# Performance work log

Hardware: AMD Instinct MI355X
Metric: run time of the kernel (lower is better)

## Reference

```python
import jax, jax.numpy as jnp
import numpy as np
from jax import lax

B, N, C, H = 8, 1024, 384, 6
D = C // H
SCALE = D ** -0.5
EPS = 1e-5


def setup_inputs() -> dict:
    key = jax.random.key(0)
    ks = jax.random.split(key, 10)
    s = 0.02
    return {
        "x": jax.random.normal(ks[0], (B, N, C), jnp.float32),
        "w_qkv": jax.random.normal(ks[1], (3 * C, C), jnp.float32) * s,
        "w_proj": jax.random.normal(ks[2], (C, C), jnp.float32) * s,
        "b_proj": jax.random.normal(ks[3], (C,), jnp.float32) * s,
        "w_kq": jax.random.normal(ks[4], (H, 1, 3, 3), jnp.float32) * 0.1,   # depthwise (groups=H)
        "b_kq": jax.random.normal(ks[5], (H,), jnp.float32) * 0.1,
        "w_head": jax.random.normal(ks[6], (H, H, 1, 1), jnp.float32) * 0.1,  # 1x1 head-mixing conv
        "b_head": jax.random.normal(ks[7], (H,), jnp.float32) * 0.1,
        "gn_w": jnp.ones((H,), jnp.float32),
        "gn_b": jnp.zeros((H,), jnp.float32),
    }


def reference(x, w_qkv, w_proj, b_proj, w_kq, b_kq, w_head, b_head, gn_w, gn_b):
    # qkv projection (torch Linear: y = x @ W.T)
    qkv = (x @ w_qkv.T).reshape(B, N, 3, H, D).transpose(2, 0, 3, 1, 4)  # [3,B,H,N,D]
    q, k, v = qkv[0], qkv[1], qkv[2]

    # attention logits [B,H,N,N]
    logits = jnp.einsum("bhnd,bhmd->bhnm", q, k) * SCALE

    # depthwise (groups=H) 3x3 conv over the NxN logit map
    logits = lax.conv_general_dilated(
        logits, w_kq, window_strides=(1, 1), padding=((1, 1), (1, 1)),
        dimension_numbers=("NCHW", "OIHW", "NCHW"), feature_group_count=H,
    ) + b_kq[None, :, None, None]

    attn = jax.nn.softmax(logits, axis=-1)

    # 1x1 conv mixing heads
    attn = jnp.einsum("oh,bhnm->bonm", w_head[:, :, 0, 0], attn) + b_head[None, :, None, None]

    # GroupNorm(num_groups=H, channels=H): per (b, head) stats over NxN
    mean = attn.mean(axis=(2, 3), keepdims=True)
    var = ((attn - mean) ** 2).mean(axis=(2, 3), keepdims=True)
    attn = (attn - mean) * lax.rsqrt(var + EPS)
    attn = attn * gn_w[None, :, None, None] + gn_b[None, :, None, None]

    out = jnp.einsum("bhnm,bhmd->bhnd", attn, v)
    out = out.transpose(0, 2, 1, 3).reshape(B, N, C)
    return out @ w_proj.T + b_proj
```

## Files before the change

### kernel.cpp

```cpp
#include <hip/hip_runtime.h>

typedef unsigned short u16;
typedef __attribute__((ext_vector_type(8))) short short8;
typedef __attribute__((ext_vector_type(4))) float f32x4;

#define MFMA(a, b, c) __builtin_amdgcn_mfma_f32_16x16x32_bf16((a), (b), (c), 0, 0, 0)

__device__ inline float bf2f(u16 u) {
  union { unsigned int i; float f; } w; w.i = ((unsigned int)u) << 16; return w.f;
}
__device__ inline u16 f2bf(float x) {
  union { float f; unsigned int i; } u; u.f = x;
  unsigned int r = u.i + 0x7fffu + ((u.i >> 16) & 1u);
  return (u16)(r >> 16);
}
__device__ inline unsigned int pk2(float a, float b) {
  return (unsigned int)f2bf(a) | ((unsigned int)f2bf(b) << 16);
}
__device__ inline void unpack8(uint4 v, float* f) {
  union { unsigned int i; float g; } c;
  c.i = v.x << 16;          f[0] = c.g;
  c.i = v.x & 0xffff0000u;  f[1] = c.g;
  c.i = v.y << 16;          f[2] = c.g;
  c.i = v.y & 0xffff0000u;  f[3] = c.g;
  c.i = v.z << 16;          f[4] = c.g;
  c.i = v.z & 0xffff0000u;  f[5] = c.g;
  c.i = v.w << 16;          f[6] = c.g;
  c.i = v.w & 0xffff0000u;  f[7] = c.g;
}

static const size_t SZ_QKV = (size_t)48 * 1024 * 64 * 2;
static const size_t SZ_MAP = (size_t)48 * 1024 * 1024 * 2;
static const size_t OFF_Q  = 0;
static const size_t OFF_K  = OFF_Q + SZ_QKV;
static const size_t OFF_VT = OFF_K + SZ_QKV;
static const size_t OFF_UG = OFF_VT + SZ_QKV;
static const size_t OFF_QM = OFF_UG + SZ_MAP;
static const size_t OFF_OT = OFF_QM + SZ_MAP;
static const size_t OFF_ST = OFF_OT + SZ_QKV;
static const size_t OFF_CS = OFF_ST + 896;

__global__ __launch_bounds__(256, 3) void k_qkv(const float* __restrict__ x,
                                                const float* __restrict__ w,
                                                u16* __restrict__ qb,
                                                u16* __restrict__ kb,
                                                u16* __restrict__ vT,
                                                float* __restrict__ colsum) {
  __shared__ u16 SH[16384];
  u16* As = SH;
  u16* Bs = SH + 8192;
  const int t = threadIdx.x;
  const int m0 = blockIdx.x * 128;
  const int n0 = blockIdx.y * 128;
  const int wave = t >> 6, lane = t & 63;
  const int wm = (wave & 1) * 64, wn = (wave >> 1) * 64;
  const int fr = lane & 15;
  const int fk = (lane >> 4) * 8;
  f32x4 acc[4][4] = {};
  for (int k0 = 0; k0 < 384; k0 += 64) {
#pragma unroll
    for (int i = 0; i < 4; ++i) {
      int e = (i * 256 + t) * 8;
      int row = e >> 6, col = e & 63;
      const float* xp = &x[(size_t)(m0 + row) * 384 + k0 + col];
      const float* wp = &w[(size_t)(n0 + row) * 384 + k0 + col];
      float4 a0 = *(const float4*)xp, a1 = *(const float4*)(xp + 4);
      uint4 av; av.x = pk2(a0.x, a0.y); av.y = pk2(a0.z, a0.w);
      av.z = pk2(a1.x, a1.y); av.w = pk2(a1.z, a1.w);
      *(uint4*)&As[e] = av;
      float4 b0 = *(const float4*)wp, b1 = *(const float4*)(wp + 4);
      uint4 bv; bv.x = pk2(b0.x, b0.y); bv.y = pk2(b0.z, b0.w);
      bv.z = pk2(b1.x, b1.y); bv.w = pk2(b1.z, b1.w);
      *(uint4*)&Bs[e] = bv;
    }
    __syncthreads();
#pragma unroll
    for (int ks = 0; ks < 2; ++ks) {
      const int ko = ks * 32 + fk;
      short8 a[4], b[4];
#pragma unroll
      for (int mi = 0; mi < 4; ++mi) a[mi] = *(const short8*)&As[(wm + mi * 16 + fr) * 64 + ko];
#pragma unroll
      for (int ni = 0; ni < 4; ++ni) b[ni] = *(const short8*)&Bs[(wn + ni * 16 + fr) * 64 + ko];
#pragma unroll
      for (int mi = 0; mi < 4; ++mi)
#pragma unroll
        for (int ni = 0; ni < 4; ++ni) acc[mi][ni] = MFMA(a[mi], b[ni], acc[mi][ni]);
    }
    __syncthreads();
  }
  u16* st = &SH[wave * 4096];
  const int gcb = n0 + wn;
  const int s = gcb / 384;
  const int remb = gcb - s * 384;
  const int h = remb >> 6;
#pragma unroll
  for (int mi = 0; mi < 4; ++mi)
#pragma unroll
    for (int ni = 0; ni < 4; ++ni)
#pragma unroll
      for (int r = 0; r < 4; ++r) {
        int rl = mi * 16 + (lane >> 4) * 4 + r;
        int cl = ni * 16 + fr;
        u16 val = f2bf(acc[mi][ni][r]);
        if (s == 2) st[cl * 64 + rl] = val;
        else        st[rl * 64 + cl] = val;
      }
  const int gm0 = m0 + wm;
  const int b_ = gm0 >> 10;
  const size_t base = (size_t)(b_ * 6 + h) << 16;
  const int nloc = gm0 & 1023;
  const int r8 = lane >> 3, c8 = (lane & 7) * 8;
#pragma unroll
  for (int i = 0; i < 8; ++i) {
    int lrow = i * 8 + r8;
    uint4 v = *(const uint4*)&st[lrow * 64 + c8];
    if (s == 0)      *(uint4*)&qb[base + (size_t)(nloc + lrow) * 64 + c8] = v;
    else if (s == 1) *(uint4*)&kb[base + (size_t)(nloc + lrow) * 64 + c8] = v;
    else             *(uint4*)&vT[base + (size_t)lrow * 1024 + nloc + c8] = v;
  }
  if (s == 2) {
#pragma unroll
    for (int ni = 0; ni < 4; ++ni) {
      float p = 0.f;
#pragma unroll
      for (int mi = 0; mi < 4; ++mi)
#pragma unroll
        for (int r = 0; r < 4; ++r) p += bf2f(f2bf(acc[mi][ni][r]));
      p += __shfl_xor(p, 16, 64);
      p += __shfl_xor(p, 32, 64);
      if ((lane >> 4) == 0)
        atomicAdd(&colsum[(b_ * 6 + h) * 64 + ni * 16 + fr], p);
    }
  }
}

__global__ __launch_bounds__(256) void k_qkconv(const u16* __restrict__ qb,
                                                const u16* __restrict__ kb,
                                                const float* __restrict__ w_kq,
                                                u16* __restrict__ Qb) {
  __shared__ u16 Sr[16 * 1040];
  __shared__ u16 Qs[16 * 68];
  __shared__ u16 Ks[64 * 68];
  __shared__ float red[4];
  const int t = threadIdx.x;
  const int bid = blockIdx.x;
  const int b_ = bid & 7;
  const int rest = bid >> 3;
  const int h = rest % 6;
  const int band = rest / 6;
  const int bh = b_ * 6 + h;
  const int n0 = band * 14;
  const int wave = t >> 6, lane = t & 63;
  const int fr = lane & 15, quad = lane >> 4;

  if (t < 128) {
    int i = t >> 3, c8 = (t & 7) * 8;
    int g = n0 - 1 + i;
    uint4 val = make_uint4(0u, 0u, 0u, 0u);
    if (g >= 0 && g < 1024)
      val = *(const uint4*)&qb[((size_t)bh << 16) + (size_t)g * 64 + c8];
    *(uint4*)&Qs[i * 68 + c8] = val;
  }
  if (t < 16) { Sr[t * 1040 + 7] = 0; Sr[t * 1040 + 1032] = 0; }
  const u16* kp = kb + ((size_t)bh << 16);
  uint4 kreg0 = *(const uint4*)&kp[(size_t)(t >> 3) * 64 + (t & 7) * 8];
  uint4 kreg1 = *(const uint4*)&kp[(size_t)(32 + (t >> 3)) * 64 + (t & 7) * 8];

  for (int c = 0; c < 16; ++c) {
    __syncthreads();
    *(uint4*)&Ks[(t >> 3) * 68 + (t & 7) * 8] = kreg0;
    *(uint4*)&Ks[((t >> 3) + 32) * 68 + (t & 7) * 8] = kreg1;
    if (c < 15) {
      const size_t ro = (size_t)(c + 1) * 64 * 64;
      kreg0 = *(const uint4*)&kp[ro + (size_t)(t >> 3) * 64 + (t & 7) * 8];
      kreg1 = *(const uint4*)&kp[ro + (size_t)(32 + (t >> 3)) * 64 + (t & 7) * 8];
    }
    __syncthreads();
    f32x4 acc = {};
#pragma unroll
    for (int ks = 0; ks < 2; ++ks) {
      short8 a = *(const short8*)&Qs[fr * 68 + ks * 32 + quad * 8];
      short8 bfr = *(const short8*)&Ks[(wave * 16 + fr) * 68 + ks * 32 + quad * 8];
      acc = MFMA(a, bfr, acc);
    }
#pragma unroll
    for (int r = 0; r < 4; ++r)
      Sr[(quad * 4 + r) * 1040 + 8 + c * 64 + wave * 16 + fr] = f2bf(acc[r] * 0.125f);
  }
  __syncthreads();

  float wv[9];
#pragma unroll
  for (int i = 0; i < 9; ++i) wv[i] = w_kq[h * 9 + i];
  const int half = t >> 7;
  const int m0 = (t & 127) * 8;
  for (int pass = 0; pass < 7; ++pass) {
    int rr = pass * 2 + half;
    float o8[8];
#pragma unroll
    for (int j = 0; j < 8; ++j) o8[j] = 0.f;
#pragma unroll
    for (int i = 0; i < 3; ++i) {
      const u16* rowp = &Sr[(rr + i) * 1040 + 8];
      float left = bf2f(rowp[m0 - 1]);
      float md[8];
      unpack8(*(const uint4*)&rowp[m0], md);
      float right = bf2f(rowp[m0 + 8]);
      float w0 = wv[i * 3 + 0], w1 = wv[i * 3 + 1], w2 = wv[i * 3 + 2];
      o8[0] += w0 * left + w1 * md[0] + w2 * md[1];
#pragma unroll
      for (int j = 1; j < 7; ++j) o8[j] += w0 * md[j - 1] + w1 * md[j] + w2 * md[j + 1];
      o8[7] += w0 * md[6] + w1 * md[7] + w2 * right;
    }
    float mx = o8[0];
#pragma unroll
    for (int j = 1; j < 8; ++j) mx = fmaxf(mx, o8[j]);
    for (int off = 32; off; off >>= 1) mx = fmaxf(mx, __shfl_xor(mx, off, 64));
    if (lane == 0) red[t >> 6] = mx;
    __syncthreads();
    float rmax = fmaxf(red[half * 2], red[half * 2 + 1]);
    __syncthreads();
    float e8[8], s = 0.f;
#pragma unroll
    for (int j = 0; j < 8; ++j) { e8[j] = __expf(o8[j] - rmax); s += e8[j]; }
    for (int off = 32; off; off >>= 1) s += __shfl_xor(s, off, 64);
    if (lane == 0) red[t >> 6] = s;
    __syncthreads();
    float rsum = red[half * 2] + red[half * 2 + 1];
    __syncthreads();
    float scale = 1024.f / rsum;
    int n = n0 + rr;
    if (n < 1024) {
      unsigned int pk[4];
#pragma unroll
      for (int jj = 0; jj < 4; ++jj)
        pk[jj] = pk2(e8[2 * jj] * scale - 1.f, e8[2 * jj + 1] * scale - 1.f);
      *(uint4*)&Qb[((size_t)bh << 20) + (size_t)n * 1024 + m0] = make_uint4(pk[0], pk[1], pk[2], pk[3]);
    }
  }
}

__global__ __launch_bounds__(256) void k_pvmix(const u16* __restrict__ Qm,
                                               const u16* __restrict__ vT,
                                               const float* __restrict__ wh,
                                               float* __restrict__ Ug,
                                               float* __restrict__ stats) {
  __shared__ u16 SH[2 * 64 * 72];
  u16* Am = SH;
  u16* Vm = SH + 64 * 72;
  const int t = threadIdx.x;
  const int bid = blockIdx.x;
  const int b_ = bid & 7;
  const int sidx = bid >> 3;
  const int n0 = (sidx / 6) * 64;
  const int o = sidx % 6;
  const int bo = b_ * 6 + o;
  const int wave = t >> 6, lane = t & 63;
  const int fr = lane & 15, quad = lane >> 4;
  const int srow = t >> 3, smg8 = (t & 7) * 8;
  float wo[6];
#pragma unroll
  for (int hh = 0; hh < 6; ++hh) wo[hh] = wh[o * 6 + hh];
  const size_t qbase = ((size_t)(b_ * 6)) << 20;
  const u16* vp = vT + ((size_t)bo << 16);
  uint4 qpre[2][6];
  uint4 vpre[2];
  {
    const int m = smg8;
#pragma unroll
    for (int i = 0; i < 2; ++i)
#pragma unroll
      for (int hh = 0; hh < 6; ++hh)
        qpre[i][hh] = *(const uint4*)&Qm[qbase + (((size_t)hh) << 20) +
                                         (size_t)(n0 + i * 32 + srow) * 1024 + m];
    vpre[0] = *(const uint4*)&vp[(size_t)srow * 1024 + m];
    vpre[1] = *(const uint4*)&vp[(size_t)(32 + srow) * 1024 + m];
  }
  f32x4 acc[4] = {};
  float s1 = 0.f, s2 = 0.f;
  for (int mc = 0; mc < 16; ++mc) {
    __syncthreads();
#pragma unroll
    for (int i = 0; i < 2; ++i) {
      float mix[8] = {0.f, 0.f, 0.f, 0.f, 0.f, 0.f, 0.f, 0.f};
#pragma unroll
      for (int hh = 0; hh < 6; ++hh) {
        float qf[8];
        unpack8(qpre[i][hh], qf);
        float w = wo[hh];
#pragma unroll
        for (int j = 0; j < 8; ++j) mix[j] += w * qf[j];
      }
#pragma unroll
      for (int j = 0; j < 8; ++j) { s1 += mix[j]; s2 += mix[j] * mix[j]; }
      uint4 pk4;
      pk4.x = pk2(mix[0], mix[1]); pk4.y = pk2(mix[2], mix[3]);
      pk4.z = pk2(mix[4], mix[5]); pk4.w = pk2(mix[6], mix[7]);
      *(uint4*)&Am[(i * 32 + srow) * 72 + smg8] = pk4;
    }
    *(uint4*)&Vm[srow * 72 + smg8] = vpre[0];
    *(uint4*)&Vm[(32 + srow) * 72 + smg8] = vpre[1];
    if (mc < 15) {
      const int m = (mc + 1) * 64 + smg8;
#pragma unroll
      for (int i = 0; i < 2; ++i)
#pragma unroll
        for (int hh = 0; hh < 6; ++hh)
          qpre[i][hh] = *(const uint4*)&Qm[qbase + (((size_t)hh) << 20) +
                                           (size_t)(n0 + i * 32 + srow) * 1024 + m];
      vpre[0] = *(const uint4*)&vp[(size_t)srow * 1024 + m];
      vpre[1] = *(const uint4*)&vp[(size_t)(32 + srow) * 1024 + m];
    }
    __syncthreads();
#pragma unroll
    for (int ks = 0; ks < 2; ++ks) {
      short8 a = *(const short8*)&Am[(wave * 16 + fr) * 72 + ks * 32 + quad * 8];
#pragma unroll
      for (int ni = 0; ni < 4; ++ni) {
        short8 b = *(const short8*)&Vm[(ni * 16 + fr) * 72 + ks * 32 + quad * 8];
        acc[ni] = MFMA(a, b, acc[ni]);
      }
    }
  }
  __syncthreads();
  float* FS = (float*)SH;
#pragma unroll
  for (int ni = 0; ni < 4; ++ni)
#pragma unroll
    for (int r = 0; r < 4; ++r)
      FS[(wave * 16 + quad * 4 + r) * 64 + ni * 16 + fr] = acc[ni][r];
  __syncthreads();
  float* Up = Ug + ((size_t)(bo * 1024 + n0)) * 64;
#pragma unroll
  for (int j = 0; j < 4; ++j) {
    int oo = j * 1024 + t * 4;
    *(float4*)&Up[oo] = *(const float4*)&FS[oo];
  }
  for (int off = 32; off; off >>= 1) {
    s1 += __shfl_xor(s1, off, 64);
    s2 += __shfl_xor(s2, off, 64);
  }
  if (lane == 0) {
    atomicAdd(&stats[bo * 2 + 0], s1);
    atomicAdd(&stats[bo * 2 + 1], s2);
  }
}

__global__ __launch_bounds__(256) void k_apply(const float* __restrict__ Ug,
                                               const float* __restrict__ stats,
                                               const float* __restrict__ colsum,
                                               const float* __restrict__ gn_w,
                                               const float* __restrict__ gn_b,
                                               u16* __restrict__ otmp) {
  int i = blockIdx.x * 256 + threadIdx.x;
  int e = i * 4;
  int d4 = e & 63;
  int n = (e >> 6) & 1023;
  int bo = e >> 16;
  int b = bo / 6, o = bo - b * 6;
  float s1 = stats[bo * 2], s2 = stats[bo * 2 + 1];
  const float inv = 1.f / 1048576.f;
  float mu = s1 * inv;
  float var = s2 * inv - mu * mu;
  float alpha = gn_w[o] * rsqrtf(var + 1e-5f * 1048576.f);
  float beta = gn_b[o] - alpha * mu;
  float4 cs = *(const float4*)&colsum[bo * 64 + d4];
  float4 u = *(const float4*)&Ug[e];
  uint2 w;
  w.x = pk2(alpha * u.x + beta * cs.x, alpha * u.y + beta * cs.y);
  w.y = pk2(alpha * u.z + beta * cs.z, alpha * u.w + beta * cs.w);
  *(uint2*)&otmp[((size_t)(b * 1024 + n)) * 384 + o * 64 + d4] = w;
}

__global__ __launch_bounds__(256, 3) void k_proj(const u16* __restrict__ A,
                                                 const float* __restrict__ w,
                                                 const float* __restrict__ bias,
                                                 float* __restrict__ out) {
  __shared__ u16 SH[16384];
  u16* As = SH;
  u16* Bs = SH + 8192;
  const int t = threadIdx.x;
  const int m0 = blockIdx.x * 128;
  const int n0 = blockIdx.y * 128;
  const int wave = t >> 6, lane = t & 63;
  const int wm = (wave & 1) * 64, wn = (wave >> 1) * 64;
  const int fr = lane & 15;
  const int fk = (lane >> 4) * 8;
  f32x4 acc[4][4] = {};
  for (int k0 = 0; k0 < 384; k0 += 64) {
#pragma unroll
    for (int i = 0; i < 4; ++i) {
      int e = (i * 256 + t) * 8;
      int row = e >> 6, col = e & 63;
      *(uint4*)&As[e] = *(const uint4*)&A[(size_t)(m0 + row) * 384 + k0 + col];
      const float* wp = &w[(size_t)(n0 + row) * 384 + k0 + col];
      float4 b0 = *(const float4*)wp, b1 = *(const float4*)(wp + 4);
      uint4 bv; bv.x = pk2(b0.x, b0.y); bv.y = pk2(b0.z, b0.w);
      bv.z = pk2(b1.x, b1.y); bv.w = pk2(b1.z, b1.w);
      *(uint4*)&Bs[e] = bv;
    }
    __syncthreads();
#pragma unroll
    for (int ks = 0; ks < 2; ++ks) {
      const int ko = ks * 32 + fk;
      short8 a[4], b[4];
#pragma unroll
      for (int mi = 0; mi < 4; ++mi) a[mi] = *(const short8*)&As[(wm + mi * 16 + fr) * 64 + ko];
#pragma unroll
      for (int ni = 0; ni < 4; ++ni) b[ni] = *(const short8*)&Bs[(wn + ni * 16 + fr) * 64 + ko];
#pragma unroll
      for (int mi = 0; mi < 4; ++mi)
#pragma unroll
        for (int ni = 0; ni < 4; ++ni) acc[mi][ni] = MFMA(a[mi], b[ni], acc[mi][ni]);
    }
    __syncthreads();
  }
  float* FS = (float*)SH;
  float* fst = &FS[wave * 2048];
  float bv[4];
#pragma unroll
  for (int ni = 0; ni < 4; ++ni) bv[ni] = bias[n0 + wn + ni * 16 + fr];
#pragma unroll
  for (int half = 0; half < 2; ++half) {
#pragma unroll
    for (int mi2 = 0; mi2 < 2; ++mi2) {
      int mi = half * 2 + mi2;
#pragma unroll
      for (int ni = 0; ni < 4; ++ni)
#pragma unroll
        for (int r = 0; r < 4; ++r)
          fst[(mi2 * 16 + (lane >> 4) * 4 + r) * 64 + ni * 16 + fr] = acc[mi][ni][r] + bv[ni];
    }
#pragma unroll
    for (int g = 0; g < 4; ++g)
#pragma unroll
      for (int i2 = 0; i2 < 2; ++i2) {
        int lrow = g * 8 + (lane >> 3);
        int colf = i2 * 32 + (lane & 7) * 4;
        float4 v = *(const float4*)&fst[lrow * 64 + colf];
        *(float4*)&out[(size_t)(m0 + wm + half * 32 + lrow) * 384 + n0 + wn + colf] = v;
      }
  }
}

extern "C" void kernel_launch(void* const* d_in, const int* in_sizes, int n_in,
                              void* d_out, int out_size, void* d_ws, size_t ws_size,
                              hipStream_t stream) {
  (void)in_sizes; (void)n_in; (void)out_size; (void)ws_size;
  const float* x      = (const float*)d_in[0];
  const float* w_qkv  = (const float*)d_in[1];
  const float* w_proj = (const float*)d_in[2];
  const float* b_proj = (const float*)d_in[3];
  const float* w_kq   = (const float*)d_in[4];
  const float* w_head = (const float*)d_in[6];
  const float* gn_w   = (const float*)d_in[8];
  const float* gn_b   = (const float*)d_in[9];

  char* ws = (char*)d_ws;
  u16*   qb      = (u16*)(ws + OFF_Q);
  u16*   kb      = (u16*)(ws + OFF_K);
  u16*   vT      = (u16*)(ws + OFF_VT);
  float* Ug      = (float*)(ws + OFF_UG);
  u16*   Qm      = (u16*)(ws + OFF_QM);
  u16*   otmp    = (u16*)(ws + OFF_OT);
  float* stats   = (float*)(ws + OFF_ST);
  float* colsum  = (float*)(ws + OFF_CS);

  hipMemsetAsync(stats, 0, 896 + 12288, stream);
  k_qkv<<<dim3(64, 9), 256, 0, stream>>>(x, w_qkv, qb, kb, vT, colsum);
  k_qkconv<<<dim3(3552), 256, 0, stream>>>(qb, kb, w_kq, Qm);
  k_pvmix<<<dim3(768), 256, 0, stream>>>(Qm, vT, w_head, Ug, stats);
  k_apply<<<dim3(3072), 256, 0, stream>>>(Ug, stats, colsum, gn_w, gn_b, otmp);
  k_proj<<<dim3(64, 3), 256, 0, stream>>>(otmp, w_proj, b_proj, (float*)d_out);
}
```

Baseline: 275.2 us.

## Use one wave per row for conv-softmax and double K chunk per barrier

The conv+softmax stage now gives each wave a whole 1024-wide row, 16 elements per lane. Row max and sum reductions therefore stay inside the wave with shuffles, removing the shared-memory reduction and four block barriers per pass. The QK logit loop loads 128 K rows per iteration instead of 64, halving the number of barrier pairs. The Sr row pitch changes to 1048. Costs are higher register pressure from the 16-wide arrays, a larger Ks tile, and idle waves on the final pass since 14 rows do not split evenly over 4 waves.

```diff
diff --git a/kernel.cpp b/kernel.cpp
--- a/kernel.cpp
+++ b/kernel.cpp
@@ -139,10 +139,9 @@
                                                 const u16* __restrict__ kb,
                                                 const float* __restrict__ w_kq,
                                                 u16* __restrict__ Qb) {
-  __shared__ u16 Sr[16 * 1040];
+  __shared__ u16 Sr[16 * 1048];
   __shared__ u16 Qs[16 * 68];
-  __shared__ u16 Ks[64 * 68];
-  __shared__ float red[4];
+  __shared__ u16 Ks[128 * 68];
   const int t = threadIdx.x;
   const int bid = blockIdx.x;
   const int b_ = bid & 7;
@@ -162,81 +161,90 @@
       val = *(const uint4*)&qb[((size_t)bh << 16) + (size_t)g * 64 + c8];
     *(uint4*)&Qs[i * 68 + c8] = val;
   }
-  if (t < 16) { Sr[t * 1040 + 7] = 0; Sr[t * 1040 + 1032] = 0; }
+  if (t < 16) { Sr[t * 1048 + 7] = 0; Sr[t * 1048 + 1032] = 0; }
   const u16* kp = kb + ((size_t)bh << 16);
-  uint4 kreg0 = *(const uint4*)&kp[(size_t)(t >> 3) * 64 + (t & 7) * 8];
-  uint4 kreg1 = *(const uint4*)&kp[(size_t)(32 + (t >> 3)) * 64 + (t & 7) * 8];
-
-  for (int c = 0; c < 16; ++c) {
-    __syncthreads();
-    *(uint4*)&Ks[(t >> 3) * 68 + (t & 7) * 8] = kreg0;
-    *(uint4*)&Ks[((t >> 3) + 32) * 68 + (t & 7) * 8] = kreg1;
-    if (c < 15) {
-      const size_t ro = (size_t)(c + 1) * 64 * 64;
-      kreg0 = *(const uint4*)&kp[ro + (size_t)(t >> 3) * 64 + (t & 7) * 8];
-      kreg1 = *(const uint4*)&kp[ro + (size_t)(32 + (t >> 3)) * 64 + (t & 7) * 8];
-    }
-    __syncthreads();
-    f32x4 acc = {};
-#pragma unroll
-    for (int ks = 0; ks < 2; ++ks) {
-      short8 a = *(const short8*)&Qs[fr * 68 + ks * 32 + quad * 8];
-      short8 bfr = *(const short8*)&Ks[(wave * 16 + fr) * 68 + ks * 32 + quad * 8];
-      acc = MFMA(a, bfr, acc);
-    }
-#pragma unroll
-    for (int r = 0; r < 4; ++r)
-      Sr[(quad * 4 + r) * 1040 + 8 + c * 64 + wave * 16 + fr] = f2bf(acc[r] * 0.125f);
+  const int krow = t >> 3, kc8 = (t & 7) * 8;
+  uint4 kreg[4];
+#pragma unroll
+  for (int j = 0; j < 4; ++j)
+    kreg[j] = *(const uint4*)&kp[(size_t)(krow + j * 32) * 64 + kc8];
+
+  for (int c = 0; c < 8; ++c) {
+    __syncthreads();
+#pragma unroll
+    for (int j = 0; j < 4; ++j)
+      *(uint4*)&Ks[(krow + j * 32) * 68 + kc8] = kreg[j];
+    if (c < 7) {
+      const size_t ro = (size_t)(c + 1) * 128 * 64;
+#pragma unroll
+      for (int j = 0; j < 4; ++j)
+        kreg[j] = *(const uint4*)&kp[ro + (size_t)(krow + j * 32) * 64 + kc8];
+    }
+    __syncthreads();
+#pragma unroll
+    for (int bf = 0; bf < 2; ++bf) {
+      f32x4 acc = {};
+#pragma unroll
+      for (int ks = 0; ks < 2; ++ks) {
+        short8 a = *(const short8*)&Qs[fr * 68 + ks * 32 + quad * 8];
+        short8 bfr = *(const short8*)&Ks[(wave * 32 + bf * 16 + fr) * 68 + ks * 32 + quad * 8];
+        acc = MFMA(a, bfr, acc);
+      }
+#pragma unroll
+      for (int r = 0; r < 4; ++r)
+        Sr[(quad * 4 + r) * 1048 + 8 + c * 128 + wave * 32 + bf * 16 + fr] = f2bf(acc[r] * 0.125f);
+    }
   }
   __syncthreads();
 
   float wv[9];
 #pragma unroll
   for (int i = 0; i < 9; ++i) wv[i] = w_kq[h * 9 + i];
-  const int half = t >> 7;
-  const int m0 = (t & 127) * 8;
-  for (int pass = 0; pass < 7; ++pass) {
-    int rr = pass * 2 + half;
-    float o8[8];
-#pragma unroll
-    for (int j = 0; j < 8; ++j) o8[j] = 0.f;
-#pragma unroll
-    for (int i = 0; i < 3; ++i) {
-      const u16* rowp = &Sr[(rr + i) * 1040 + 8];
-      float left = bf2f(rowp[m0 - 1]);
-      float md[8];
-      unpack8(*(const uint4*)&rowp[m0], md);
-      float right = bf2f(rowp[m0 + 8]);
-      float w0 = wv[i * 3 + 0], w1 = wv[i * 3 + 1], w2 = wv[i * 3 + 2];
-      o8[0] += w0 * left + w1 * md[0] + w2 * md[1];
-#pragma unroll
-      for (int j = 1; j < 7; ++j) o8[j] += w0 * md[j - 1] + w1 * md[j] + w2 * md[j + 1];
-      o8[7] += w0 * md[6] + w1 * md[7] + w2 * right;
-    }
-    float mx = o8[0];
-#pragma unroll
-    for (int j = 1; j < 8; ++j) mx = fmaxf(mx, o8[j]);
-    for (int off = 32; off; off >>= 1) mx = fmaxf(mx, __shfl_xor(mx, off, 64));
-    if (lane == 0) red[t >> 6] = mx;
-    __syncthreads();
-    float rmax = fmaxf(red[half * 2], red[half * 2 + 1]);
-    __syncthreads();
-    float e8[8], s = 0.f;
-#pragma unroll
-    for (int j = 0; j < 8; ++j) { e8[j] = __expf(o8[j] - rmax); s += e8[j]; }
-    for (int off = 32; off; off >>= 1) s += __shfl_xor(s, off, 64);
-    if (lane == 0) red[t >> 6] = s;
-    __syncthreads();
-    float rsum = red[half * 2] + red[half * 2 + 1];
-    __syncthreads();
-    float scale = 1024.f / rsum;
+  const int c0 = lane * 16;
+  for (int pass = 0; pass < 4; ++pass) {
+    int rr = pass * 4 + wave;
     int n = n0 + rr;
-    if (n < 1024) {
-      unsigned int pk[4];
-#pragma unroll
-      for (int jj = 0; jj < 4; ++jj)
-        pk[jj] = pk2(e8[2 * jj] * scale - 1.f, e8[2 * jj + 1] * scale - 1.f);
-      *(uint4*)&Qb[((size_t)bh << 20) + (size_t)n * 1024 + m0] = make_uint4(pk[0], pk[1], pk[2], pk[3]);
+    if (rr < 14 && n < 1024) {
+      float o16[16];
+#pragma unroll
+      for (int j = 0; j < 16; ++j) o16[j] = 0.f;
+#pragma unroll
+      for (int i = 0; i < 3; ++i) {
+        const u16* rowp = &Sr[(rr + i) * 1048 + 8];
+        float md[16];
+        unpack8(*(const uint4*)&rowp[c0], md);
+        unpack8(*(const uint4*)&rowp[c0 + 8], md + 8);
+        float left  = bf2f(rowp[c0 - 1]);
+        float right = bf2f(rowp[c0 + 16]);
+        float w0 = wv[i * 3 + 0], w1 = wv[i * 3 + 1], w2 = wv[i * 3 + 2];
+        o16[0] += w0 * left + w1 * md[0] + w2 * md[1];
+#pragma unroll
+        for (int j = 1; j < 15; ++j) o16[j] += w0 * md[j - 1] + w1 * md[j] + w2 * md[j + 1];
+        o16[15] += w0 * md[14] + w1 * md[15] + w2 * right;
+      }
+      float mx = o16[0];
+#pragma unroll
+      for (int j = 1; j < 16; ++j) mx = fmaxf(mx, o16[j]);
+#pragma unroll
+      for (int off = 32; off; off >>= 1) mx = fmaxf(mx, __shfl_xor(mx, off, 64));
+      float e16[16], s = 0.f;
+#pragma unroll
+      for (int j = 0; j < 16; ++j) { e16[j] = __expf(o16[j] - mx); s += e16[j]; }
+#pragma unroll
+      for (int off = 32; off; off >>= 1) s += __shfl_xor(s, off, 64);
+      float scale = 1024.f / s;
+      uint4 p0, p1;
+      p0.x = pk2(e16[0] * scale - 1.f,  e16[1] * scale - 1.f);
+      p0.y = pk2(e16[2] * scale - 1.f,  e16[3] * scale - 1.f);
+      p0.z = pk2(e16[4] * scale - 1.f,  e16[5] * scale - 1.f);
+      p0.w = pk2(e16[6] * scale - 1.f,  e16[7] * scale - 1.f);
+      p1.x = pk2(e16[8] * scale - 1.f,  e16[9] * scale - 1.f);
+      p1.y = pk2(e16[10] * scale - 1.f, e16[11] * scale - 1.f);
+      p1.z = pk2(e16[12] * scale - 1.f, e16[13] * scale - 1.f);
+      p1.w = pk2(e16[14] * scale - 1.f, e16[15] * scale - 1.f);
+      u16* dst = &Qb[((size_t)bh << 20) + (size_t)n * 1024 + c0];
+      *(uint4*)&dst[0] = p0;
+      *(uint4*)&dst[8] = p1;
     }
   }
 }
```

Measured after the change: 324.8 us. +18.0%, slower.
